# Performance work log

Measured on AMD Instinct MI355X. Metric: run time of the kernel, lower is better.

The kernel has to match this reference:

```python
import jax, jax.numpy as jnp
import numpy as np

B, L, H, NH = 2, 1024, 768, 12
NE, M, NC, CW = 24, 3, 2, 8
BLOCK, NCLS = 64, 97
OFFSET = 1  # bert cls offset


def setup_inputs() -> dict:
    key = jax.random.key(0)
    ks = jax.random.split(key, 10)
    s = 0.02
    return {
        "sequence_output": jax.random.normal(ks[0], (B, L, H), jnp.float32),
        "attention": jax.random.uniform(ks[1], (B, NH, L, L), jnp.float32),
        "mention_starts": jax.random.randint(ks[2], (B, NE, M), 0, L - 2),
        "coref_starts": jax.random.randint(ks[3], (B, NE, NC), 0, L - CW),
        "W_head": jax.random.normal(ks[4], (H, 2 * H), jnp.float32) * s,
        "b_head": jnp.zeros((H,), jnp.float32),
        "W_tail": jax.random.normal(ks[5], (H, 2 * H), jnp.float32) * s,
        "b_tail": jnp.zeros((H,), jnp.float32),
        "W_proj": jax.random.normal(ks[6], (H, H * BLOCK), jnp.float32) * s,
        "W_cls": jax.random.normal(ks[7], (NCLS, H), jnp.float32) * s,
        "b_cls": jnp.zeros((NCLS,), jnp.float32),
    }


def reference(sequence_output, attention, mention_starts, coref_starts,
              W_head, b_head, W_tail, b_tail, W_proj, W_cls, b_cls):
    # ---- get_hrt (NoGraphConv/NoKGEmbedding => graph feats are zeros; residual=True) ----
    p = mention_starts + OFFSET                              # [B,NE,M]
    bidx = jnp.arange(B)[:, None, None]
    m_emb = sequence_output[bidx, p]                         # [B,NE,M,H]
    # attention[i,:,pos] gathered for every mention -> [B,NE,M,NH,L]
    m_att = attention[bidx, :, p]

    # gated coref: gate_score = mean-over-mentions, sum-over-heads, normalized
    att = m_att.mean(2).sum(2)                               # [B,NE,L]
    gate = att / att.sum(-1, keepdims=True)                  # [B,NE,L]

    widx = coref_starts[..., None] + jnp.arange(CW)          # [B,NE,NC,CW]
    gate_g = jnp.take_along_axis(gate[:, :, None, :], widx, axis=-1)   # [B,NE,NC,CW]
    seq_g = sequence_output[jnp.arange(B)[:, None, None, None], widx]  # [B,NE,NC,CW,H]
    coref_emb = (gate_g[..., None] * seq_g).sum(3)           # [B,NE,NC,H]

    # entity embedding: logsumexp over mentions + gated coref vectors
    e_emb = jax.nn.logsumexp(jnp.concatenate([m_emb, coref_emb], axis=2), axis=2)  # [B,NE,H]
    e_att = m_att.mean(2)                                    # [B,NE,NH,L]

    # head-tail localized context: relu((h_att*t_att).sum(heads)), normalize, mix tokens
    ht = jax.nn.relu(jnp.einsum('behl,bfhl->befl', e_att, e_att))      # [B,NE,NE,L]
    ht = ht / (ht.sum(-1, keepdims=True) + 1e-10)
    rs = jnp.einsum('befl,bld->befd', ht, sequence_output)   # [B,NE,NE,H]

    hs = jnp.broadcast_to(e_emb[:, :, None, :], (B, NE, NE, H))
    ts = jnp.broadcast_to(e_emb[:, None, :, :], (B, NE, NE, H))

    # ---- extractors + grouped bilinear + projection + classifier ----
    zh = jnp.tanh(jnp.concatenate([hs, rs], -1) @ W_head.T + b_head)   # [B,NE,NE,H]
    zt = jnp.tanh(jnp.concatenate([ts, rs], -1) @ W_tail.T + b_tail)
    K = H // BLOCK
    b1 = zh.reshape(B, NE, NE, K, BLOCK)
    b2 = zt.reshape(B, NE, NE, K, BLOCK)
    bl = (b1[..., :, None] * b2[..., None, :]).reshape(B, NE, NE, H * BLOCK)
    feature = bl @ W_proj.T                                  # [B,NE,NE,H] (NoAxialTransformer adds zeros)
    logits = feature @ W_cls.T + b_cls                       # [B,NE,NE,NCLS]
    return logits
```

## Files before the change

kernel.cpp:

```cpp
#include <hip/hip_runtime.h>
#include <math.h>

#define BB   2
#define LL   1024
#define HH   768
#define NHH  12
#define NEE  24
#define MMM  3
#define NCC  2
#define CWW  8
#define BLK  64
#define NCLS 97
#define HB   49152
#define NCP  128
#define NCT  7
#define NEF  1152

typedef unsigned int uint;
typedef unsigned short ushort;
typedef __attribute__((ext_vector_type(8))) short bf16x8;
typedef __attribute__((ext_vector_type(4))) float f32x4;

__device__ __forceinline__ ushort f2bf(float f) {
    uint u = __float_as_uint(f);
    u += 0x7fffu + ((u >> 16) & 1u);
    return (ushort)(u >> 16);
}

__device__ __forceinline__ void splitbf(float f, ushort& h, ushort& l) {
    h = f2bf(f);
    float hf = __uint_as_float((uint)h << 16);
    l = f2bf(f - hf);
}

__global__ void k_front(const float* __restrict__ att_in, const float* __restrict__ seq,
                        const int* __restrict__ ms, const int* __restrict__ cs,
                        const float* __restrict__ Wc, const float* __restrict__ Wh,
                        const float* __restrict__ Wt, const float* __restrict__ bc,
                        float* __restrict__ e_att, float* __restrict__ e_emb,
                        ushort* __restrict__ wcpack,
                        ushort* __restrict__ seqThi, ushort* __restrict__ seqTlo,
                        ushort* __restrict__ W2hi, ushort* __restrict__ W2lo,
                        float* __restrict__ out) {
    __shared__ float sm[13328];
    int bid = blockIdx.x;
    int tid = threadIdx.x;
    if (bid < 42) {
        int t = bid * 256 + tid;
        if (t >= 24 * NCT * 64) return;
        int kc = t / (NCT * 64);
        int r = t % (NCT * 64);
        int ct = r >> 6;
        int lane = r & 63;
        int c = ct * 16 + (lane & 15);
        int k0 = kc * 32 + (lane >> 4) * 8;
        uint u[4] = {0u, 0u, 0u, 0u};
        if (c < NCLS) {
            const float* src = Wc + (size_t)c * HH + k0;
            float4 f0 = *(const float4*)src;
            float4 f1 = *(const float4*)(src + 4);
            u[0] = (uint)f2bf(f0.x) | ((uint)f2bf(f0.y) << 16);
            u[1] = (uint)f2bf(f0.z) | ((uint)f2bf(f0.w) << 16);
            u[2] = (uint)f2bf(f1.x) | ((uint)f2bf(f1.y) << 16);
            u[3] = (uint)f2bf(f1.z) | ((uint)f2bf(f1.w) << 16);
        }
        *(uint4*)(wcpack + (size_t)t * 8) = make_uint4(u[0], u[1], u[2], u[3]);
    } else if (bid < 479) {
        int i = (bid - 42) * 256 + tid;
        if (i < NEF * NCLS) out[i] = bc[i % NCLS];
    } else if (bid < 527) {
        float* es = sm;
        float* gs = sm + 12288;
        float* red = sm + 13312;
        int be = bid - 479;
        int b = be / NEE;
        int base = be * MMM;
        int p0 = ms[base + 0] + 1, p1 = ms[base + 1] + 1, p2 = ms[base + 2] + 1;
        float* eo = e_att + (size_t)be * NHH * LL;
        for (int h = 0; h < NHH; h++) {
            const float* basep = att_in + (size_t)(b * NHH + h) * LL * LL;
#pragma unroll
            for (int i = 0; i < 4; i++) {
                int l = tid + i * 256;
                float v = (basep[(size_t)p0 * LL + l] + basep[(size_t)p1 * LL + l] +
                           basep[(size_t)p2 * LL + l]) * (1.f / 3.f);
                es[h * LL + l] = v;
                eo[h * LL + l] = v;
            }
        }
        __syncthreads();
        float part = 0.f;
#pragma unroll
        for (int i = 0; i < 4; i++) {
            int l = tid + i * 256;
            float a = 0.f;
#pragma unroll
            for (int h = 0; h < NHH; h++) a += es[h * LL + l];
            gs[l] = a;
            part += a;
        }
        for (int off = 32; off; off >>= 1) part += __shfl_down(part, off, 64);
        if ((tid & 63) == 0) red[tid >> 6] = part;
        __syncthreads();
        float inv = 1.f / (red[0] + red[1] + red[2] + red[3]);
#pragma unroll
        for (int i = 0; i < 4; i++) gs[tid + i * 256] *= inv;
        __syncthreads();
        int c0 = cs[be * NCC + 0], c1 = cs[be * NCC + 1];
        for (int d = tid; d < HH; d += 256) {
            float v0 = seq[((size_t)b * LL + p0) * HH + d];
            float v1 = seq[((size_t)b * LL + p1) * HH + d];
            float v2 = seq[((size_t)b * LL + p2) * HH + d];
            float s0 = 0.f, s1 = 0.f;
#pragma unroll
            for (int w = 0; w < CWW; w++) {
                s0 += gs[c0 + w] * seq[((size_t)b * LL + c0 + w) * HH + d];
                s1 += gs[c1 + w] * seq[((size_t)b * LL + c1 + w) * HH + d];
            }
            float mx = fmaxf(fmaxf(fmaxf(v0, v1), fmaxf(v2, s0)), s1);
            float se = expf(v0 - mx) + expf(v1 - mx) + expf(v2 - mx) + expf(s0 - mx) + expf(s1 - mx);
            e_emb[(size_t)be * HH + d] = logf(se) + mx;
        }
    } else if (bid < 911) {
        float (*tile)[65] = (float(*)[65])sm;
        int idx = bid - 527;
        int b = idx / 192;
        int rem = idx % 192;
        int l0 = (rem / 12) * 64;
        int d0 = (rem % 12) * 64;
        int dq = tid >> 6, dl = tid & 63;
#pragma unroll 4
        for (int r = 0; r < 16; r++) {
            int l_in = r * 4 + dq;
            tile[l_in][dl] = seq[((size_t)(b * LL + l0 + l_in)) * HH + d0 + dl];
        }
        __syncthreads();
#pragma unroll 4
        for (int r = 0; r < 16; r++) {
            int d_out = r * 4 + dq;
            float v = tile[dl][d_out];
            ushort h, l;
            splitbf(v, h, l);
            size_t o = ((size_t)(b * HH + d0 + d_out)) * LL + l0 + dl;
            seqThi[o] = h;
            seqTlo[o] = l;
        }
    } else {
        int idx = bid - 911;
#pragma unroll
        for (int rr = 0; rr < 4; rr++) {
            int n = idx * 4 + rr;
            const float* src = (n < HH) ? (Wh + (size_t)n * (2 * HH) + HH)
                                        : (Wt + (size_t)(n - HH) * (2 * HH) + HH);
            for (int k = tid; k < HH; k += 256) {
                ushort h, l;
                splitbf(src[k], h, l);
                W2hi[(size_t)n * HH + k] = h;
                W2lo[(size_t)n * HH + k] = l;
            }
        }
    }
}

__global__ void k_htwf(const float* __restrict__ e_att, const float* __restrict__ Wp,
                       const ushort* __restrict__ wcpack, ushort* __restrict__ hthi,
                       ushort* __restrict__ htlo, ushort* __restrict__ bpack) {
    __shared__ float hts[LL];
    __shared__ float red[4];
    int bid = blockIdx.x;
    int tid = threadIdx.x;
    int lane = tid & 63, w = tid >> 6;
    if (bid < 768) {
        int r16 = lane & 15, tt = lane >> 4;
        int n0 = bid * 64 + w * 16;
        const float* ap = Wp + (size_t)(tt * 8) * HB + n0 + r16;
        const uint4* wb = (const uint4*)wcpack;
        f32x4 acc[NCT];
        f32x4 zero = {0.f, 0.f, 0.f, 0.f};
#pragma unroll
        for (int ct = 0; ct < NCT; ct++) acc[ct] = zero;
        for (int kc = 0; kc < 24; kc++) {
            const float* a0 = ap + (size_t)(kc * 32) * HB;
            float f[8];
#pragma unroll
            for (int j = 0; j < 8; j++) f[j] = a0[(size_t)j * HB];
            union { bf16x8 v; uint u[4]; } a;
#pragma unroll
            for (int q = 0; q < 4; q++)
                a.u[q] = (__float_as_uint(f[2 * q]) >> 16) |
                         (__float_as_uint(f[2 * q + 1]) & 0xFFFF0000u);
#pragma unroll
            for (int ct = 0; ct < NCT; ct++) {
                union { uint4 q; bf16x8 v; } b;
                b.q = wb[(size_t)(kc * NCT + ct) * 64 + lane];
                acc[ct] = __builtin_amdgcn_mfma_f32_16x16x32_bf16(a.v, b.v, acc[ct], 0, 0, 0);
            }
        }
#pragma unroll
        for (int ct = 0; ct < NCT; ct++) {
            int c = ct * 16 + r16;
#pragma unroll
            for (int r = 0; r < 4; r++) {
                int n = n0 + tt * 4 + r;
                bpack[((size_t)(n >> 3) * NCP + c) * 8 + (n & 7)] = f2bf(acc[ct][r]);
            }
        }
    } else {
        int blk = bid - 768;
        int f = blk % NEE;
        int e = (blk / NEE) % NEE;
        int b = blk / (NEE * NEE);
        const float* ea = e_att + (size_t)(b * NEE + e) * NHH * LL;
        const float* fa = e_att + (size_t)(b * NEE + f) * NHH * LL;
        float lsum = 0.f;
        for (int l = tid; l < LL; l += 256) {
            float s = 0.f;
            for (int h = 0; h < NHH; h++) s += ea[h * LL + l] * fa[h * LL + l];
            s = fmaxf(s, 0.f);
            hts[l] = s;
            lsum += s;
        }
        for (int off = 32; off; off >>= 1) lsum += __shfl_down(lsum, off, 64);
        if ((tid & 63) == 0) red[tid >> 6] = lsum;
        __syncthreads();
        float inv = 1.f / (red[0] + red[1] + red[2] + red[3] + 1e-10f);
        for (int l = tid; l < LL; l += 256) {
            ushort h, lo;
            splitbf(hts[l] * inv, h, lo);
            hthi[(size_t)blk * LL + l] = h;
            htlo[(size_t)blk * LL + l] = lo;
        }
    }
}

__global__ void k_mid(const ushort* __restrict__ seqThi, const ushort* __restrict__ seqTlo,
                      const ushort* __restrict__ hthi, const ushort* __restrict__ htlo,
                      const float* __restrict__ e_emb, const float* __restrict__ Wh,
                      const float* __restrict__ Wt, ushort* __restrict__ rshi,
                      ushort* __restrict__ rslo, float* __restrict__ hsW,
                      float* __restrict__ tsW) {
    __shared__ float xs[HH];
    int bid = blockIdx.x;
    int tid = threadIdx.x;
    int lane = tid & 63, w = tid >> 6;
    if (bid < 216) {
        int b = bid / 108;
        int rem = bid % 108;
        int m0 = (rem / 12) * 64;
        int n0 = (rem % 12) * 64;
        int r16 = lane & 15, tt = lane >> 4;
        const ushort* Ah = hthi + (size_t)(b * 576 + m0 + w * 16 + r16) * LL;
        const ushort* Al = htlo + (size_t)(b * 576 + m0 + w * 16 + r16) * LL;
        const ushort* Bh0 = seqThi + (size_t)(b * HH + n0 + r16) * LL;
        const ushort* Bl0 = seqTlo + (size_t)(b * HH + n0 + r16) * LL;
        f32x4 acc[4];
        f32x4 zero = {0.f, 0.f, 0.f, 0.f};
#pragma unroll
        for (int nt = 0; nt < 4; nt++) acc[nt] = zero;
        for (int kc = 0; kc < 32; kc++) {
            int ko = kc * 32 + tt * 8;
            bf16x8 ah = *(const bf16x8*)(Ah + ko);
            bf16x8 al = *(const bf16x8*)(Al + ko);
#pragma unroll
            for (int nt = 0; nt < 4; nt++) {
                bf16x8 bh = *(const bf16x8*)(Bh0 + (size_t)nt * 16 * LL + ko);
                bf16x8 bl = *(const bf16x8*)(Bl0 + (size_t)nt * 16 * LL + ko);
                acc[nt] = __builtin_amdgcn_mfma_f32_16x16x32_bf16(ah, bh, acc[nt], 0, 0, 0);
                acc[nt] = __builtin_amdgcn_mfma_f32_16x16x32_bf16(ah, bl, acc[nt], 0, 0, 0);
                acc[nt] = __builtin_amdgcn_mfma_f32_16x16x32_bf16(al, bh, acc[nt], 0, 0, 0);
            }
        }
#pragma unroll
        for (int nt = 0; nt < 4; nt++) {
#pragma unroll
            for (int r = 0; r < 4; r++) {
                int m = b * 576 + m0 + w * 16 + tt * 4 + r;
                int d = n0 + nt * 16 + r16;
                ushort h, l;
                splitbf(acc[nt][r], h, l);
                rshi[(size_t)m * HH + d] = h;
                rslo[(size_t)m * HH + d] = l;
            }
        }
    } else {
        int r = bid - 216;
        int m2 = r % 48;
        int which = (r / 48) & 1;
        int chunk = r / 96;
        const float* Wm = which ? Wt : Wh;
        float* outp = which ? tsW : hsW;
        const float* x = e_emb + (size_t)m2 * HH;
        for (int j = tid; j < HH; j += 256) xs[j] = x[j];
        __syncthreads();
        int d0 = chunk * 64 + w * 16;
#pragma unroll 4
        for (int i = 0; i < 16; i++) {
            int d = d0 + i;
            const float* wr = Wm + (size_t)d * (2 * HH);
            float s = 0.f;
#pragma unroll
            for (int jj = 0; jj < 12; jj++) s += xs[lane + jj * 64] * wr[lane + jj * 64];
            for (int off = 32; off; off >>= 1) s += __shfl_down(s, off, 64);
            if (lane == 0) outp[(size_t)m2 * HH + d] = s;
        }
    }
}

__global__ void k_rsw(const ushort* __restrict__ rshi, const ushort* __restrict__ rslo,
                      const ushort* __restrict__ W2hi, const ushort* __restrict__ W2lo,
                      const float* __restrict__ hsW, const float* __restrict__ tsW,
                      const float* __restrict__ bh, const float* __restrict__ bt,
                      ushort* __restrict__ zb) {
    int m0 = blockIdx.x * 64, n0 = blockIdx.y * 64;
    int tid = threadIdx.x;
    int lane = tid & 63, w = tid >> 6;
    int r16 = lane & 15, tt = lane >> 4;
    const ushort* Ah = rshi + (size_t)(m0 + w * 16 + r16) * HH;
    const ushort* Al = rslo + (size_t)(m0 + w * 16 + r16) * HH;
    const ushort* Bh0 = W2hi + (size_t)(n0 + r16) * HH;
    const ushort* Bl0 = W2lo + (size_t)(n0 + r16) * HH;
    f32x4 acc[4];
    f32x4 zero = {0.f, 0.f, 0.f, 0.f};
#pragma unroll
    for (int nt = 0; nt < 4; nt++) acc[nt] = zero;
    for (int kc = 0; kc < 24; kc++) {
        int ko = kc * 32 + tt * 8;
        bf16x8 ah = *(const bf16x8*)(Ah + ko);
        bf16x8 al = *(const bf16x8*)(Al + ko);
#pragma unroll
        for (int nt = 0; nt < 4; nt++) {
            bf16x8 vbh = *(const bf16x8*)(Bh0 + (size_t)nt * 16 * HH + ko);
            bf16x8 vbl = *(const bf16x8*)(Bl0 + (size_t)nt * 16 * HH + ko);
            acc[nt] = __builtin_amdgcn_mfma_f32_16x16x32_bf16(ah, vbh, acc[nt], 0, 0, 0);
            acc[nt] = __builtin_amdgcn_mfma_f32_16x16x32_bf16(ah, vbl, acc[nt], 0, 0, 0);
            acc[nt] = __builtin_amdgcn_mfma_f32_16x16x32_bf16(al, vbh, acc[nt], 0, 0, 0);
        }
    }
    bool isHead = (n0 < HH);
    const float* bias = isHead ? bh : bt;
#pragma unroll
    for (int nt = 0; nt < 4; nt++) {
#pragma unroll
        for (int r = 0; r < 4; r++) {
            int m = m0 + w * 16 + tt * 4 + r;
            int n = n0 + nt * 16 + r16;
            int bb = m / 576;
            int rr = m % 576;
            int e = rr / NEE, f = rr % NEE;
            int d = isHead ? n : (n - HH);
            const float* addrow = isHead ? (hsW + (size_t)(bb * NEE + e) * HH)
                                         : (tsW + (size_t)(bb * NEE + f) * HH);
            float v = tanhf(acc[nt][r] + addrow[d] + bias[d]);
            zb[(size_t)m * (2 * HH) + n] = f2bf(v);
        }
    }
}

#define ZTP 88
#define ZHP 48
__global__ __launch_bounds__(256, 2) void k_logits(const ushort* __restrict__ zb,
                                                   const ushort* __restrict__ bpack,
                                                   float* __restrict__ out) {
    __shared__ ushort zhs[64 * ZHP];
    __shared__ ushort zts[64 * ZTP];
    __shared__ ushort Bls[16384];
    int m0 = blockIdx.x * 64;
    int kb = blockIdx.y;
    int kg = kb >> 1;
    int ihalf = (kb & 1) * 32;
    int tid = threadIdx.x;
    int lane = tid & 63, w = tid >> 6;
    int tt = lane >> 4, r16 = lane & 15;
    int wm = (w & 1) * 32, wn = (w >> 1) * 64;

    {
        int row = tid >> 2, c8 = (tid & 3) * 16;
        const ushort* src = zb + (size_t)(m0 + row) * 1536 + 768 + kg * 64 + c8;
        uint4 v0 = *(const uint4*)src;
        uint4 v1 = *(const uint4*)(src + 8);
        *(uint4*)&zts[row * ZTP + c8] = v0;
        *(uint4*)&zts[row * ZTP + c8 + 8] = v1;
    }
    {
        int row = tid >> 2, c8 = (tid & 3) * 8;
        const ushort* src = zb + (size_t)(m0 + row) * 1536 + kg * 64 + ihalf + c8;
        *(uint4*)&zhs[row * ZHP + c8] = *(const uint4*)src;
    }

    f32x4 acc[2][4];
    f32x4 zero = {0.f, 0.f, 0.f, 0.f};
#pragma unroll
    for (int t = 0; t < 2; t++)
#pragma unroll
        for (int n = 0; n < 4; n++) acc[t][n] = zero;

    const char* bbase = (const char*)bpack + (size_t)kb * 2048 * 256;
    for (int g = 0; g < 16; g++) {
        __syncthreads();
        const char* sb = bbase + (size_t)g * 32768;
#pragma unroll
        for (int q = 0; q < 8; q++) {
            int off = (q * 4 + w) * 1024;
            __builtin_amdgcn_global_load_lds(
                (const __attribute__((address_space(1))) void*)(sb + off + lane * 16),
                (__attribute__((address_space(3))) void*)((char*)Bls + off),
                16, 0, 0);
        }
        __syncthreads();
#pragma unroll
        for (int ks = 0; ks < 4; ks++) {
            int s = g * 4 + ks;
            int il = s >> 1;
            int j0 = (s & 1) * 32;
            bf16x8 af[2];
#pragma unroll
            for (int t = 0; t < 2; t++) {
                int row = wm + t * 16 + r16;
                float zhf = __uint_as_float((uint)zhs[row * ZHP + il] << 16);
                union { bf16x8 v; uint u[4]; } zt8, a;
                zt8.v = *(const bf16x8*)&zts[row * ZTP + j0 + tt * 8];
#pragma unroll
                for (int q = 0; q < 4; q++) {
                    uint p = zt8.u[q];
                    uint lo = __float_as_uint(__uint_as_float(p << 16) * zhf);
                    uint hi = __float_as_uint(__uint_as_float(p & 0xFFFF0000u) * zhf);
                    a.u[q] = (lo >> 16) | (hi & 0xFFFF0000u);
                }
                af[t] = a.v;
            }
#pragma unroll
            for (int n = 0; n < 4; n++) {
                bf16x8 bf = *(const bf16x8*)&Bls[(size_t)((ks * 4 + tt) * NCP + wn + n * 16 + r16) * 8];
                acc[0][n] = __builtin_amdgcn_mfma_f32_16x16x32_bf16(af[0], bf, acc[0][n], 0, 0, 0);
                acc[1][n] = __builtin_amdgcn_mfma_f32_16x16x32_bf16(af[1], bf, acc[1][n], 0, 0, 0);
            }
        }
    }
    int rbase = (lane >> 4) * 4;
#pragma unroll
    for (int t = 0; t < 2; t++)
#pragma unroll
        for (int n = 0; n < 4; n++) {
            int c = wn + n * 16 + r16;
            if (c < NCLS) {
                int row = m0 + wm + t * 16 + rbase;
#pragma unroll
                for (int r = 0; r < 4; r++)
                    atomicAdd(&out[(size_t)(row + r) * NCLS + c], acc[t][n][r]);
            }
        }
}

extern "C" void kernel_launch(void* const* d_in, const int* in_sizes, int n_in,
                              void* d_out, int out_size, void* d_ws, size_t ws_size,
                              hipStream_t stream) {
    const float* seq  = (const float*)d_in[0];
    const float* attn = (const float*)d_in[1];
    const int*   ms   = (const int*)d_in[2];
    const int*   cs   = (const int*)d_in[3];
    const float* Wh   = (const float*)d_in[4];
    const float* bh   = (const float*)d_in[5];
    const float* Wt   = (const float*)d_in[6];
    const float* bt   = (const float*)d_in[7];
    const float* Wp   = (const float*)d_in[8];
    const float* Wc   = (const float*)d_in[9];
    const float* bc   = (const float*)d_in[10];
    float* out = (float*)d_out;

    float* w     = (float*)d_ws;
    float* e_att = w;
    float* eemb  = e_att + 589824;
    float* hsW   = eemb + 36864;
    float* tsW   = hsW + 36864;
    ushort* seqThi = (ushort*)(tsW + 36864);
    ushort* seqTlo = seqThi + 1572864;
    ushort* W2hi   = seqTlo + 1572864;
    ushort* W2lo   = W2hi + 1179648;
    ushort* hthi   = W2lo + 1179648;
    ushort* htlo   = hthi + 1179648;
    ushort* rshi   = htlo + 1179648;
    ushort* rslo   = rshi + 884736;
    ushort* zb     = rslo + 884736;
    ushort* wcpack = zb + 1769472;
    ushort* bpack  = wcpack + 86016;

    k_front<<<1295, 256, 0, stream>>>(attn, seq, ms, cs, Wc, Wh, Wt, bc,
                                      e_att, eemb, wcpack, seqThi, seqTlo, W2hi, W2lo, out);
    k_htwf<<<1920, 256, 0, stream>>>(e_att, Wp, wcpack, hthi, htlo, bpack);
    k_mid<<<1368, 256, 0, stream>>>(seqThi, seqTlo, hthi, htlo, eemb, Wh, Wt,
                                    rshi, rslo, hsW, tsW);
    k_rsw<<<dim3(18, 24), 256, 0, stream>>>(rshi, rslo, W2hi, W2lo, hsW, tsW, bh, bt, zb);
    k_logits<<<dim3(18, 24), 256, 0, stream>>>(zb, bpack, out);
}
```

Measured before the change: 447.8 us.

## Stage W_proj tiles through LDS, halve k_mid blocks, pre-expand z to fp32 in k_logits

k_htwf now loads each W_proj k-chunk into shared memory with coalesced global_load_lds and then reads the strided rows from LDS, instead of doing strided global loads per lane. k_mid runs with 128-thread blocks and twice as many blocks, each covering half the rows, to improve load balance and occupancy. k_logits converts the z tiles to fp32 once in LDS, using an XOR swizzle to avoid bank conflicts, and builds the bf16 products with v_cvt_pk_bf16_f32. This cuts per-iteration unpacking, at the cost of more LDS use and extra syncs per chunk in k_htwf. The cvt instruction rounds to nearest, where the old code truncated.

```diff
diff --git a/kernel.cpp b/kernel.cpp
--- a/kernel.cpp
+++ b/kernel.cpp
@@ -165,25 +165,34 @@
 __global__ void k_htwf(const float* __restrict__ e_att, const float* __restrict__ Wp,
                        const ushort* __restrict__ wcpack, ushort* __restrict__ hthi,
                        ushort* __restrict__ htlo, ushort* __restrict__ bpack) {
-    __shared__ float hts[LL];
-    __shared__ float red[4];
+    __shared__ float smem[2052];
     int bid = blockIdx.x;
     int tid = threadIdx.x;
     int lane = tid & 63, w = tid >> 6;
     if (bid < 768) {
         int r16 = lane & 15, tt = lane >> 4;
-        int n0 = bid * 64 + w * 16;
-        const float* ap = Wp + (size_t)(tt * 8) * HB + n0 + r16;
+        int n0 = bid * 64;
         const uint4* wb = (const uint4*)wcpack;
         f32x4 acc[NCT];
         f32x4 zero = {0.f, 0.f, 0.f, 0.f};
 #pragma unroll
         for (int ct = 0; ct < NCT; ct++) acc[ct] = zero;
         for (int kc = 0; kc < 24; kc++) {
-            const float* a0 = ap + (size_t)(kc * 32) * HB;
+#pragma unroll
+            for (int q = 0; q < 2; q++) {
+                int base = q * 256 + w * 64;
+                int srow = (base + lane) >> 4;
+                int scol = ((base + lane) & 15) * 4;
+                __builtin_amdgcn_global_load_lds(
+                    (const __attribute__((address_space(1))) void*)
+                        (Wp + (size_t)(kc * 32 + srow) * HB + n0 + scol),
+                    (__attribute__((address_space(3))) void*)((char*)smem + base * 16),
+                    16, 0, 0);
+            }
+            __syncthreads();
             float f[8];
 #pragma unroll
-            for (int j = 0; j < 8; j++) f[j] = a0[(size_t)j * HB];
+            for (int j = 0; j < 8; j++) f[j] = smem[(tt * 8 + j) * 64 + w * 16 + r16];
             union { bf16x8 v; uint u[4]; } a;
 #pragma unroll
             for (int q = 0; q < 4; q++)
@@ -195,17 +204,20 @@
                 b.q = wb[(size_t)(kc * NCT + ct) * 64 + lane];
                 acc[ct] = __builtin_amdgcn_mfma_f32_16x16x32_bf16(a.v, b.v, acc[ct], 0, 0, 0);
             }
+            __syncthreads();
         }
 #pragma unroll
         for (int ct = 0; ct < NCT; ct++) {
             int c = ct * 16 + r16;
 #pragma unroll
             for (int r = 0; r < 4; r++) {
-                int n = n0 + tt * 4 + r;
+                int n = n0 + w * 16 + tt * 4 + r;
                 bpack[((size_t)(n >> 3) * NCP + c) * 8 + (n & 7)] = f2bf(acc[ct][r]);
             }
         }
     } else {
+        float* hts = smem;
+        float* red = smem + 1024;
         int blk = bid - 768;
         int f = blk % NEE;
         int e = (blk / NEE) % NEE;
@@ -243,10 +255,10 @@
     int bid = blockIdx.x;
     int tid = threadIdx.x;
     int lane = tid & 63, w = tid >> 6;
-    if (bid < 216) {
-        int b = bid / 108;
-        int rem = bid % 108;
-        int m0 = (rem / 12) * 64;
+    if (bid < 432) {
+        int b = bid / 216;
+        int rem = bid % 216;
+        int m0 = (rem / 12) * 32;
         int n0 = (rem % 12) * 64;
         int r16 = lane & 15, tt = lane >> 4;
         const ushort* Ah = hthi + (size_t)(b * 576 + m0 + w * 16 + r16) * LL;
@@ -283,16 +295,16 @@
             }
         }
     } else {
-        int r = bid - 216;
+        int r = bid - 432;
         int m2 = r % 48;
         int which = (r / 48) & 1;
         int chunk = r / 96;
         const float* Wm = which ? Wt : Wh;
         float* outp = which ? tsW : hsW;
         const float* x = e_emb + (size_t)m2 * HH;
-        for (int j = tid; j < HH; j += 256) xs[j] = x[j];
-        __syncthreads();
-        int d0 = chunk * 64 + w * 16;
+        for (int j = tid; j < HH; j += 128) xs[j] = x[j];
+        __syncthreads();
+        int d0 = chunk * 32 + w * 16;
 #pragma unroll 4
         for (int i = 0; i < 16; i++) {
             int d = d0 + i;
@@ -356,13 +368,11 @@
     }
 }
 
-#define ZTP 88
-#define ZHP 48
 __global__ __launch_bounds__(256, 2) void k_logits(const ushort* __restrict__ zb,
                                                    const ushort* __restrict__ bpack,
                                                    float* __restrict__ out) {
-    __shared__ ushort zhs[64 * ZHP];
-    __shared__ ushort zts[64 * ZTP];
+    __shared__ float zhs_f[64 * 33];
+    __shared__ float zts_f[64 * 64];
     __shared__ ushort Bls[16384];
     int m0 = blockIdx.x * 64;
     int kb = blockIdx.y;
@@ -374,17 +384,34 @@
     int wm = (w & 1) * 32, wn = (w >> 1) * 64;
 
     {
-        int row = tid >> 2, c8 = (tid & 3) * 16;
-        const ushort* src = zb + (size_t)(m0 + row) * 1536 + 768 + kg * 64 + c8;
+        int row = tid >> 2, c0 = (tid & 3) * 16;
+        const ushort* src = zb + (size_t)(m0 + row) * 1536 + 768 + kg * 64 + c0;
         uint4 v0 = *(const uint4*)src;
         uint4 v1 = *(const uint4*)(src + 8);
-        *(uint4*)&zts[row * ZTP + c8] = v0;
-        *(uint4*)&zts[row * ZTP + c8 + 8] = v1;
+        uint uu[8] = {v0.x, v0.y, v0.z, v0.w, v1.x, v1.y, v1.z, v1.w};
+        char* dst = (char*)zts_f + row * 256;
+        int sw = (row & 7) << 4;
+#pragma unroll
+        for (int s = 0; s < 4; s++) {
+            float4 fv;
+            fv.x = __uint_as_float(uu[2 * s] << 16);
+            fv.y = __uint_as_float(uu[2 * s] & 0xFFFF0000u);
+            fv.z = __uint_as_float(uu[2 * s + 1] << 16);
+            fv.w = __uint_as_float(uu[2 * s + 1] & 0xFFFF0000u);
+            *(float4*)(dst + ((c0 * 4 + s * 16) ^ sw)) = fv;
+        }
     }
     {
-        int row = tid >> 2, c8 = (tid & 3) * 8;
-        const ushort* src = zb + (size_t)(m0 + row) * 1536 + kg * 64 + ihalf + c8;
-        *(uint4*)&zhs[row * ZHP + c8] = *(const uint4*)src;
+        int row = tid >> 2, c0 = (tid & 3) * 8;
+        const ushort* src = zb + (size_t)(m0 + row) * 1536 + kg * 64 + ihalf + c0;
+        uint4 v = *(const uint4*)src;
+        uint uu[4] = {v.x, v.y, v.z, v.w};
+        float* dst = zhs_f + row * 33 + c0;
+#pragma unroll
+        for (int s = 0; s < 4; s++) {
+            dst[2 * s]     = __uint_as_float(uu[s] << 16);
+            dst[2 * s + 1] = __uint_as_float(uu[s] & 0xFFFF0000u);
+        }
     }
 
     f32x4 acc[2][4];
@@ -416,16 +443,21 @@
 #pragma unroll
             for (int t = 0; t < 2; t++) {
                 int row = wm + t * 16 + r16;
-                float zhf = __uint_as_float((uint)zhs[row * ZHP + il] << 16);
-                union { bf16x8 v; uint u[4]; } zt8, a;
-                zt8.v = *(const bf16x8*)&zts[row * ZTP + j0 + tt * 8];
-#pragma unroll
-                for (int q = 0; q < 4; q++) {
-                    uint p = zt8.u[q];
-                    uint lo = __float_as_uint(__uint_as_float(p << 16) * zhf);
-                    uint hi = __float_as_uint(__uint_as_float(p & 0xFFFF0000u) * zhf);
-                    a.u[q] = (lo >> 16) | (hi & 0xFFFF0000u);
-                }
+                float zhf = zhs_f[row * 33 + il];
+                const char* zbase = (const char*)zts_f + row * 256;
+                int sw = (row & 7) << 4;
+                int b0 = (j0 + tt * 8) * 4;
+                f32x4 zlo = *(const f32x4*)(zbase + (b0 ^ sw));
+                f32x4 zhi = *(const f32x4*)(zbase + ((b0 + 16) ^ sw));
+                float p0 = zlo[0] * zhf, p1 = zlo[1] * zhf;
+                float p2 = zlo[2] * zhf, p3 = zlo[3] * zhf;
+                float p4 = zhi[0] * zhf, p5 = zhi[1] * zhf;
+                float p6 = zhi[2] * zhf, p7 = zhi[3] * zhf;
+                union { bf16x8 v; uint u[4]; } a;
+                asm("v_cvt_pk_bf16_f32 %0, %1, %2" : "=v"(a.u[0]) : "v"(p0), "v"(p1));
+                asm("v_cvt_pk_bf16_f32 %0, %1, %2" : "=v"(a.u[1]) : "v"(p2), "v"(p3));
+                asm("v_cvt_pk_bf16_f32 %0, %1, %2" : "=v"(a.u[2]) : "v"(p4), "v"(p5));
+                asm("v_cvt_pk_bf16_f32 %0, %1, %2" : "=v"(a.u[3]) : "v"(p6), "v"(p7));
                 af[t] = a.v;
             }
 #pragma unroll
@@ -487,7 +519,7 @@
     k_front<<<1295, 256, 0, stream>>>(attn, seq, ms, cs, Wc, Wh, Wt, bc,
                                       e_att, eemb, wcpack, seqThi, seqTlo, W2hi, W2lo, out);
     k_htwf<<<1920, 256, 0, stream>>>(e_att, Wp, wcpack, hthi, htlo, bpack);
-    k_mid<<<1368, 256, 0, stream>>>(seqThi, seqTlo, hthi, htlo, eemb, Wh, Wt,
+    k_mid<<<2736, 128, 0, stream>>>(seqThi, seqTlo, hthi, htlo, eemb, Wh, Wt,
                                     rshi, rslo, hsW, tsW);
     k_rsw<<<dim3(18, 24), 256, 0, stream>>>(rshi, rslo, W2hi, W2lo, hsW, tsW, bh, bt, zb);
     k_logits<<<dim3(18, 24), 256, 0, stream>>>(zb, bpack, out);
```

Result: no change. 448.3 us (+0.1%).
